# Performance work log

Hardware: AMD Instinct MI355X
Metric: run time of the kernel (lower is better)

The kernel has to match this reference:

```python
import jax, jax.numpy as jnp
import numpy as np

SEQ, BATCH, D_MODEL = 2048, 2, 1024
NHEAD = 16
HEAD_DIM = D_MODEL // NHEAD
D_FF = 4096
LN_EPS = 1e-5
ROPE_THETA = 10000.0


def _rope_cos_sin(seq_len, dim, dtype):
    # lucidrains RotaryEmbedding: inv_freq over even indices, interleaved repeat
    inv_freq = 1.0 / (ROPE_THETA ** (jnp.arange(0, dim, 2, dtype=jnp.float32) / dim))
    t = jnp.arange(seq_len, dtype=jnp.float32)
    freqs = t[:, None] * inv_freq[None, :]            # [S, dim/2]
    freqs = jnp.repeat(freqs, 2, axis=-1)             # [S, dim] (f0,f0,f1,f1,...)
    return jnp.cos(freqs).astype(dtype), jnp.sin(freqs).astype(dtype)


def _rotate_half(x):
    # interleaved pairs: (x0,x1,x2,x3,...) -> (-x1,x0,-x3,x2,...)
    x = x.reshape(x.shape[:-1] + (-1, 2))
    x1, x2 = x[..., 0], x[..., 1]
    return jnp.stack([-x2, x1], axis=-1).reshape(x.shape[:-2] + (-1,))


def _apply_rope(x, cos, sin):
    # x: [B, H, S, D]; cos/sin: [S, D]
    return x * cos[None, None, :, :] + _rotate_half(x) * sin[None, None, :, :]


def _layer_norm(x, g, b):
    mu = jnp.mean(x, axis=-1, keepdims=True)
    var = jnp.mean(jnp.square(x - mu), axis=-1, keepdims=True)
    return (x - mu) * jax.lax.rsqrt(var + LN_EPS) * g + b


def setup_inputs() -> dict:
    key = jax.random.key(0)
    ks = jax.random.split(key, 12)
    s = 1.0 / np.sqrt(D_MODEL)
    sf = 1.0 / np.sqrt(D_FF)
    return {
        "src": jax.random.normal(ks[0], (SEQ, BATCH, D_MODEL), jnp.float32),
        "q_w": jax.random.uniform(ks[1], (D_MODEL, D_MODEL), jnp.float32, -s, s),
        "q_b": jnp.zeros((D_MODEL,), jnp.float32),
        "k_w": jax.random.uniform(ks[2], (D_MODEL, D_MODEL), jnp.float32, -s, s),
        "k_b": jnp.zeros((D_MODEL,), jnp.float32),
        "v_w": jax.random.uniform(ks[3], (D_MODEL, D_MODEL), jnp.float32, -s, s),
        "v_b": jnp.zeros((D_MODEL,), jnp.float32),
        "w1": jax.random.uniform(ks[4], (D_MODEL, D_FF), jnp.float32, -s, s),
        "b1": jnp.zeros((D_FF,), jnp.float32),
        "w2": jax.random.uniform(ks[5], (D_FF, D_MODEL), jnp.float32, -sf, sf),
        "b2": jnp.zeros((D_MODEL,), jnp.float32),
        "ln1_g": jnp.ones((D_MODEL,), jnp.float32),
        "ln1_b": jnp.zeros((D_MODEL,), jnp.float32),
        "ln2_g": jnp.ones((D_MODEL,), jnp.float32),
        "ln2_b": jnp.zeros((D_MODEL,), jnp.float32),
    }


def reference(src, q_w, q_b, k_w, k_b, v_w, v_b, w1, b1, w2, b2,
              ln1_g, ln1_b, ln2_g, ln2_b):
    S, B, E = src.shape
    q = src @ q_w + q_b
    k = src @ k_w + k_b
    v = src @ v_w + v_b
    # [S,B,E] -> [B,H,S,D]
    def split_heads(x):
        return x.reshape(S, B, NHEAD, HEAD_DIM).transpose(1, 2, 0, 3)
    q, k, v = split_heads(q), split_heads(k), split_heads(v)
    cos, sin = _rope_cos_sin(S, HEAD_DIM, src.dtype)
    q = _apply_rope(q, cos, sin)
    k = _apply_rope(k, cos, sin)
    scores = jnp.einsum("bhqd,bhkd->bhqk", q, k) / np.sqrt(HEAD_DIM)
    probs = jax.nn.softmax(scores, axis=-1)
    out = jnp.einsum("bhqk,bhkd->bhqd", probs, v)      # [B,H,S,D]
    out = out.transpose(2, 0, 1, 3).reshape(S, B, E)
    x = _layer_norm(src + out, ln1_g, ln1_b)
    ff = (jax.nn.relu(x @ w1 + b1)) @ w2 + b2
    return _layer_norm(x + ff, ln2_g, ln2_b)
```

## Files before the change

### kernel.cpp

```cpp
#include <hip/hip_runtime.h>
#include <hip/hip_bf16.h>

#define SEQ 2048
#define BATCH 2
#define DMODEL 1024
#define NHEAD 16
#define HDIM 64
#define DFF 4096
#define LN_EPS 1e-5f
#define QKVSZ (BATCH * NHEAD * SEQ * HDIM)

typedef unsigned short ushort_t;
typedef __attribute__((ext_vector_type(8))) short short8;
typedef __attribute__((ext_vector_type(4))) float floatx4;

__device__ __forceinline__ float bf2f(ushort_t u) {
    union { unsigned int i; float f; } v;
    v.i = ((unsigned int)u) << 16;
    return v.f;
}
__device__ __forceinline__ ushort_t f2bf(float f) {
    union { float f; unsigned int i; } v;
    v.f = f;
    unsigned int r = v.i + 0x7fffu + ((v.i >> 16) & 1u);
    return (ushort_t)(r >> 16);
}
__device__ __forceinline__ void gload_lds16(const ushort_t* g, ushort_t* l) {
    __builtin_amdgcn_global_load_lds(
        (const __attribute__((address_space(1))) void*)g,
        (__attribute__((address_space(3))) void*)l, 16, 0, 0);
}

__global__ __launch_bounds__(256) void sniff_kernel(const ushort_t* __restrict__ qw,
                                                    int* __restrict__ flag) {
    float mx = 0.f;
    for (int i = threadIdx.x; i < 4096; i += 256) {
        float v = fabsf(bf2f(qw[i]));
        if (v <= 3.0e38f) mx = fmaxf(mx, v);
    }
#pragma unroll
    for (int off = 1; off < 64; off <<= 1) mx = fmaxf(mx, __shfl_xor(mx, off, 64));
    __shared__ float sm[4];
    if ((threadIdx.x & 63) == 0) sm[threadIdx.x >> 6] = mx;
    __syncthreads();
    if (threadIdx.x == 0) {
        float m = fmaxf(fmaxf(sm[0], sm[1]), fmaxf(sm[2], sm[3]));
        *flag = (m > 1.0f) ? 1 : 0;
    }
}

__global__ __launch_bounds__(256) void convert_kernel(const void* __restrict__ src,
                                                      ushort_t* __restrict__ dst,
                                                      int n, const int* __restrict__ flag) {
    const int f = *flag;
    int i = blockIdx.x * 256 + threadIdx.x;
    const int stride = gridDim.x * 256;
    if (f) {
        const float* s = (const float*)src;
        for (; i < n; i += stride) dst[i] = f2bf(s[i]);
    } else {
        const ushort_t* s = (const ushort_t*)src;
        for (; i < n; i += stride) dst[i] = s[i];
    }
}

__global__ __launch_bounds__(256) void transpose_all_kernel(
    const void* __restrict__ s0, const void* __restrict__ s1,
    const void* __restrict__ s2, const void* __restrict__ s3,
    const void* __restrict__ s4,
    ushort_t* __restrict__ wqkvT, ushort_t* __restrict__ w1T,
    ushort_t* __restrict__ w2T, const int* __restrict__ flag)
{
    __shared__ ushort_t tile[64][72];
    const int id = blockIdx.x;
    const void* src; ushort_t* dst; int K, N, bx, by;
    if (id < 768) {
        int mat = id >> 8, t = id & 255;
        src = (mat == 0) ? s0 : ((mat == 1) ? s1 : s2);
        dst = wqkvT + (size_t)mat * DMODEL * DMODEL;
        K = DMODEL; N = DMODEL; bx = t & 15; by = t >> 4;
    } else if (id < 1792) {
        int t = id - 768;
        src = s3; dst = w1T; K = DMODEL; N = DFF; bx = t & 63; by = t >> 6;
    } else {
        int t = id - 1792;
        src = s4; dst = w2T; K = DFF; N = DMODEL; bx = t & 15; by = t >> 4;
    }
    const int n0 = bx * 64, k0 = by * 64;
    const int tx = threadIdx.x & 63, ty = threadIdx.x >> 6;
    const int f = *flag;
    if (f) {
        const float* s = (const float*)src;
#pragma unroll
        for (int i = 0; i < 16; i++) {
            int r = ty + 4 * i;
            tile[r][tx] = f2bf(s[(size_t)(k0 + r) * N + n0 + tx]);
        }
    } else {
        const ushort_t* s = (const ushort_t*)src;
#pragma unroll
        for (int i = 0; i < 16; i++) {
            int r = ty + 4 * i;
            tile[r][tx] = s[(size_t)(k0 + r) * N + n0 + tx];
        }
    }
    __syncthreads();
#pragma unroll
    for (int i = 0; i < 16; i++) {
        int r = ty + 4 * i;
        dst[(size_t)(n0 + r) * K + k0 + tx] = tile[tx][r];
    }
}

__global__ __launch_bounds__(256) void small_setup_kernel(
    const void* __restrict__ qb, const void* __restrict__ kb,
    const void* __restrict__ vb, const void* __restrict__ b1,
    const void* __restrict__ b2, const void* __restrict__ g1,
    const void* __restrict__ be1, const void* __restrict__ g2,
    const void* __restrict__ be2,
    char* __restrict__ sp, float* __restrict__ rope,
    const int* __restrict__ flag)
{
    const int i = blockIdx.x * 256 + threadIdx.x;
    if (i >= 12288) {
        int idx = i - 12288;
        int s = idx >> 5, ii = idx & 31;
        float inv = exp2f(-(float)(2 * ii) * (13.287712379549449f / 64.f));
        float ang = (float)s * inv;
        rope[idx * 2 + 0] = cosf(ang);
        rope[idx * 2 + 1] = sinf(ang);
        return;
    }
    const int f = *flag;
    const void* src; ushort_t* dst; int j;
    if (i < 3072)       { src = (i < 1024) ? qb : ((i < 2048) ? kb : vb);
                          j = i & 1023; dst = (ushort_t*)sp + i; }
    else if (i < 7168)  { src = b1;  j = i - 3072;  dst = (ushort_t*)(sp + 8192) + j; }
    else if (i < 8192)  { src = b2;  j = i - 7168;  dst = (ushort_t*)(sp + 16384) + j; }
    else if (i < 9216)  { src = g1;  j = i - 8192;  dst = (ushort_t*)(sp + 20480) + j; }
    else if (i < 10240) { src = be1; j = i - 9216;  dst = (ushort_t*)(sp + 24576) + j; }
    else if (i < 11264) { src = g2;  j = i - 10240; dst = (ushort_t*)(sp + 28672) + j; }
    else                { src = be2; j = i - 11264; dst = (ushort_t*)(sp + 32768) + j; }
    *dst = f ? f2bf(((const float*)src)[j]) : ((const ushort_t*)src)[j];
}

template <int MODE>
__global__ __launch_bounds__(256) void gemm_kernel(
    const ushort_t* __restrict__ A, const ushort_t* __restrict__ BT,
    const ushort_t* __restrict__ bias, void* __restrict__ out,
    void* __restrict__ out2, const float* __restrict__ rope,
    int M, int N, int K)
{
    __shared__ ushort_t sA[128 * 32];
    __shared__ ushort_t sB[128 * 32];

    const int tid = threadIdx.x;
    const int lane = tid & 63;
    const int w = tid >> 6;
    const int wm = (w >> 1) * 64;
    const int wn = (w & 1) * 64;
    const int m0 = blockIdx.y * 128;
    const int n0 = blockIdx.x * 128;

    const int Kc = (MODE == 3) ? (K >> 1) : K;
    const int kbeg = (MODE == 3) ? (int)blockIdx.z * Kc : 0;

    floatx4 acc[4][4];
#pragma unroll
    for (int i = 0; i < 4; i++)
#pragma unroll
        for (int j = 0; j < 4; j++) {
            floatx4 z = {0.f, 0.f, 0.f, 0.f};
            acc[i][j] = z;
        }

    const int srow = tid >> 2;
    const int scol = (tid & 3) * 8;
    const ushort_t* Ag = A + (size_t)(m0 + srow) * K + scol + kbeg;
    const ushort_t* Bg = BT + (size_t)(n0 + srow) * K + scol + kbeg;
    ushort_t* ldsA0 = sA + w * 512;
    ushort_t* ldsA1 = sA + 2048 + w * 512;
    ushort_t* ldsB0 = sB + w * 512;
    ushort_t* ldsB1 = sB + 2048 + w * 512;
    const size_t rstep = (size_t)64 * K;

    for (int k0 = 0; k0 < Kc; k0 += 32) {
        gload_lds16(Ag + k0, ldsA0);
        gload_lds16(Ag + rstep + k0, ldsA1);
        gload_lds16(Bg + k0, ldsB0);
        gload_lds16(Bg + rstep + k0, ldsB1);
        __syncthreads();

        short8 a[4], b[4];
#pragma unroll
        for (int mt = 0; mt < 4; mt++)
            a[mt] = *(const short8*)&sA[(wm + mt * 16 + (lane & 15)) * 32 + (lane >> 4) * 8];
#pragma unroll
        for (int nt = 0; nt < 4; nt++)
            b[nt] = *(const short8*)&sB[(wn + nt * 16 + (lane & 15)) * 32 + (lane >> 4) * 8];
#pragma unroll
        for (int mt = 0; mt < 4; mt++)
#pragma unroll
            for (int nt = 0; nt < 4; nt++)
                acc[mt][nt] = __builtin_amdgcn_mfma_f32_16x16x32_bf16(
                    a[mt], b[nt], acc[mt][nt], 0, 0, 0);
        __syncthreads();
    }

#pragma unroll
    for (int mt = 0; mt < 4; mt++) {
#pragma unroll
        for (int nt = 0; nt < 4; nt++) {
#pragma unroll
            for (int r = 0; r < 4; r++) {
                int row = wm + mt * 16 + (lane >> 4) * 4 + r;
                int col = wn + nt * 16 + (lane & 15);
                int m = m0 + row, n = n0 + col;
                float val = acc[mt][nt][r];
                if (MODE != 3) val += bf2f(bias[n]);
                if (MODE == 1) {
                    int mat = n >> 10, nn = n & 1023;
                    int h = nn >> 6, d = nn & 63;
                    int s = m >> 1, bb = m & 1;
                    if (mat < 2) {
                        int i = d >> 1;
                        float c  = rope[((size_t)s * 32 + i) * 2 + 0];
                        float sn = rope[((size_t)s * 32 + i) * 2 + 1];
                        float partner = __shfl_xor(val, 1, 64);
                        val = (d & 1) ? (val * c + partner * sn)
                                      : (val * c - partner * sn);
                        if (mat == 0) val *= 0.18033688011112042f;
                    }
                    size_t off;
                    if (mat == 2)
                        off = (size_t)2 * QKVSZ + ((size_t)(bb * NHEAD + h) * HDIM + d) * SEQ + s;
                    else
                        off = (size_t)mat * QKVSZ + ((size_t)(bb * NHEAD + h) * SEQ + s) * HDIM + d;
                    ((ushort_t*)out)[off] = f2bf(val);
                } else if (MODE == 2) {
                    ((ushort_t*)out)[(size_t)m * N + n] = f2bf(fmaxf(val, 0.f));
                } else {
                    float* outp = blockIdx.z ? (float*)out2 : (float*)out;
                    outp[(size_t)m * N + n] = val;
                }
            }
        }
    }
}

__global__ __launch_bounds__(256) void attn_kernel(
    const ushort_t* __restrict__ Q, const ushort_t* __restrict__ K,
    const ushort_t* __restrict__ VT, ushort_t* __restrict__ out)
{
    __shared__ ushort_t sQ[128][72];
    __shared__ ushort_t sK[64][72];
    __shared__ ushort_t sVT[64][72];
    __shared__ ushort_t sP[128][72];

    const int tid = threadIdx.x;
    const int lane = tid & 63;
    const int w = tid >> 6;
    const int quad = lane >> 4;
    const int l15 = lane & 15;
    const int bh = blockIdx.y;
    const int q0 = blockIdx.x * 128;

    const ushort_t* Qg  = Q + ((size_t)bh * SEQ + q0) * HDIM;
    const ushort_t* Kg  = K + (size_t)bh * SEQ * HDIM;
    const ushort_t* VTg = VT + (size_t)bh * SEQ * HDIM;

#pragma unroll
    for (int p = 0; p < 4; p++) {
        int chunk = tid + p * 256;
        int r = chunk >> 3, c = (chunk & 7) * 8;
        *(short8*)&sQ[r][c] = *(const short8*)(Qg + (size_t)r * HDIM + c);
    }
    __syncthreads();
    short8 aQ[2][2];
#pragma unroll
    for (int mt = 0; mt < 2; mt++)
#pragma unroll
        for (int kk = 0; kk < 2; kk++)
            aQ[mt][kk] = *(const short8*)&sQ[w * 32 + mt * 16 + l15][kk * 32 + quad * 8];

    floatx4 accO[2][4];
    floatx4 accL[2];
#pragma unroll
    for (int mt = 0; mt < 2; mt++) {
        floatx4 z = {0.f, 0.f, 0.f, 0.f};
        accL[mt] = z;
#pragma unroll
        for (int nt = 0; nt < 4; nt++) accO[mt][nt] = z;
    }
    short8 ones;
#pragma unroll
    for (int j = 0; j < 8; j++) ones[j] = (short)0x3F80;

    for (int kv0 = 0; kv0 < SEQ; kv0 += 64) {
        __syncthreads();
#pragma unroll
        for (int p = 0; p < 2; p++) {
            int chunk = tid + p * 256;
            int r = chunk >> 3, c = (chunk & 7) * 8;
            *(short8*)&sK[r][c]  = *(const short8*)(Kg + (size_t)(kv0 + r) * HDIM + c);
            *(short8*)&sVT[r][c] = *(const short8*)(VTg + (size_t)r * SEQ + kv0 + c);
        }
        __syncthreads();

        floatx4 accS[2][4];
#pragma unroll
        for (int mt = 0; mt < 2; mt++)
#pragma unroll
            for (int nt = 0; nt < 4; nt++) {
                floatx4 z = {0.f, 0.f, 0.f, 0.f};
                accS[mt][nt] = z;
            }
#pragma unroll
        for (int kk = 0; kk < 2; kk++)
#pragma unroll
            for (int nt = 0; nt < 4; nt++) {
                short8 bK = *(const short8*)&sK[nt * 16 + l15][kk * 32 + quad * 8];
#pragma unroll
                for (int mt = 0; mt < 2; mt++)
                    accS[mt][nt] = __builtin_amdgcn_mfma_f32_16x16x32_bf16(
                        aQ[mt][kk], bK, accS[mt][nt], 0, 0, 0);
            }

#pragma unroll
        for (int mt = 0; mt < 2; mt++)
#pragma unroll
            for (int nt = 0; nt < 4; nt++)
#pragma unroll
                for (int r = 0; r < 4; r++)
                    sP[w * 32 + mt * 16 + quad * 4 + r][nt * 16 + l15] =
                        f2bf(exp2f(accS[mt][nt][r]));

#pragma unroll
        for (int mt = 0; mt < 2; mt++) {
#pragma unroll
            for (int kkp = 0; kkp < 2; kkp++) {
                short8 aP = *(const short8*)&sP[w * 32 + mt * 16 + l15][kkp * 32 + quad * 8];
#pragma unroll
                for (int nt = 0; nt < 4; nt++) {
                    short8 bV = *(const short8*)&sVT[nt * 16 + l15][kkp * 32 + quad * 8];
                    accO[mt][nt] = __builtin_amdgcn_mfma_f32_16x16x32_bf16(
                        aP, bV, accO[mt][nt], 0, 0, 0);
                }
                accL[mt] = __builtin_amdgcn_mfma_f32_16x16x32_bf16(
                    aP, ones, accL[mt], 0, 0, 0);
            }
        }
    }

    const int b = bh >> 4, h = bh & 15;
#pragma unroll
    for (int mt = 0; mt < 2; mt++) {
        float rinv[4];
#pragma unroll
        for (int r = 0; r < 4; r++) rinv[r] = 1.0f / accL[mt][r];
#pragma unroll
        for (int nt = 0; nt < 4; nt++)
#pragma unroll
            for (int r = 0; r < 4; r++) {
                int qrow = q0 + w * 32 + mt * 16 + quad * 4 + r;
                int d = nt * 16 + l15;
                out[((size_t)qrow * BATCH + b) * DMODEL + h * HDIM + d] =
                    f2bf(accO[mt][nt][r] * rinv[r]);
            }
    }
}

__global__ __launch_bounds__(256) void ln1_kernel(
    const ushort_t* __restrict__ src, ushort_t* io,
    const ushort_t* __restrict__ g, const ushort_t* __restrict__ bb)
{
    const int row = blockIdx.x;
    const int tid = threadIdx.x;
    const size_t base = (size_t)row * DMODEL;
    const int j0 = tid * 4;
    float v[4];
#pragma unroll
    for (int j = 0; j < 4; j++)
        v[j] = bf2f(src[base + j0 + j]) + bf2f(io[base + j0 + j]);

    float s = v[0] + v[1] + v[2] + v[3];
    float ss = v[0] * v[0] + v[1] * v[1] + v[2] * v[2] + v[3] * v[3];
#pragma unroll
    for (int off = 1; off < 64; off <<= 1) {
        s += __shfl_xor(s, off, 64);
        ss += __shfl_xor(ss, off, 64);
    }
    __shared__ float ps[4], pss[4];
    if ((tid & 63) == 0) { ps[tid >> 6] = s; pss[tid >> 6] = ss; }
    __syncthreads();
    s = ps[0] + ps[1] + ps[2] + ps[3];
    ss = pss[0] + pss[1] + pss[2] + pss[3];
    float mu = s * (1.f / DMODEL);
    float var = ss * (1.f / DMODEL) - mu * mu;
    float rstd = rsqrtf(var + LN_EPS);
#pragma unroll
    for (int j = 0; j < 4; j++) {
        float y = (v[j] - mu) * rstd * bf2f(g[j0 + j]) + bf2f(bb[j0 + j]);
        io[base + j0 + j] = f2bf(y);
    }
}

__global__ __launch_bounds__(256) void ln2_kernel(
    const ushort_t* __restrict__ xb, float* io,
    const float* __restrict__ ff1, const ushort_t* __restrict__ b2,
    const ushort_t* __restrict__ g, const ushort_t* __restrict__ bb)
{
    const int row = blockIdx.x;
    const int tid = threadIdx.x;
    const size_t base = (size_t)row * DMODEL;
    const int j0 = tid * 4;
    float v[4];
#pragma unroll
    for (int j = 0; j < 4; j++)
        v[j] = bf2f(xb[base + j0 + j]) + io[base + j0 + j] + ff1[base + j0 + j]
             + bf2f(b2[j0 + j]);

    float s = v[0] + v[1] + v[2] + v[3];
    float ss = v[0] * v[0] + v[1] * v[1] + v[2] * v[2] + v[3] * v[3];
#pragma unroll
    for (int off = 1; off < 64; off <<= 1) {
        s += __shfl_xor(s, off, 64);
        ss += __shfl_xor(ss, off, 64);
    }
    __shared__ float ps[4], pss[4];
    if ((tid & 63) == 0) { ps[tid >> 6] = s; pss[tid >> 6] = ss; }
    __syncthreads();
    s = ps[0] + ps[1] + ps[2] + ps[3];
    ss = pss[0] + pss[1] + pss[2] + pss[3];
    float mu = s * (1.f / DMODEL);
    float var = ss * (1.f / DMODEL) - mu * mu;
    float rstd = rsqrtf(var + LN_EPS);
#pragma unroll
    for (int j = 0; j < 4; j++) {
        float y = (v[j] - mu) * rstd * bf2f(g[j0 + j]) + bf2f(bb[j0 + j]);
        io[base + j0 + j] = y;
    }
}

extern "C" void kernel_launch(void* const* d_in, const int* in_sizes, int n_in,
                              void* d_out, int out_size, void* d_ws, size_t ws_size,
                              hipStream_t stream)
{
    char* ws = (char*)d_ws;
    const size_t MB = 1024 * 1024;
    const size_t KB = 1024;

    ushort_t* c_src   = (ushort_t*)(ws + 0);
    ushort_t* c_wqkvT = (ushort_t*)(ws + 8 * MB);
    ushort_t* c_w1T   = (ushort_t*)(ws + 14 * MB);
    ushort_t* c_w2T   = (ushort_t*)(ws + 22 * MB);
    char* sp = ws + 30 * MB;
    ushort_t* c_qkvb  = (ushort_t*)(sp + 0 * KB);
    ushort_t* c_b1    = (ushort_t*)(sp + 8 * KB);
    ushort_t* c_b2    = (ushort_t*)(sp + 16 * KB);
    ushort_t* c_ln1g  = (ushort_t*)(sp + 20 * KB);
    ushort_t* c_ln1b  = (ushort_t*)(sp + 24 * KB);
    ushort_t* c_ln2g  = (ushort_t*)(sp + 28 * KB);
    ushort_t* c_ln2b  = (ushort_t*)(sp + 32 * KB);
    int*      flag    = (int*)(sp + 36 * KB);
    float*    rope    = (float*)(ws + 30 * MB + 512 * KB);
    ushort_t* QKVb    = (ushort_t*)(ws + 31 * MB);
    ushort_t* attn_xb = (ushort_t*)(ws + 63 * MB);
    ushort_t* hbuf    = (ushort_t*)(ws + 31 * MB);
    float*    ffb1    = (float*)(ws + 0);
    float*    ffb0    = (float*)d_out;

    const int M = SEQ * BATCH;
    dim3 blk(256);

    sniff_kernel<<<dim3(1), blk, 0, stream>>>((const ushort_t*)d_in[1], flag);

    transpose_all_kernel<<<dim3(2816), blk, 0, stream>>>(
        d_in[1], d_in[3], d_in[5], d_in[7], d_in[9],
        c_wqkvT, c_w1T, c_w2T, flag);

    convert_kernel<<<dim3(2048), blk, 0, stream>>>(
        d_in[0], c_src, SEQ * BATCH * DMODEL, flag);

    small_setup_kernel<<<dim3(304), blk, 0, stream>>>(
        d_in[2], d_in[4], d_in[6], d_in[8], d_in[10],
        d_in[11], d_in[12], d_in[13], d_in[14],
        sp, rope, flag);

    gemm_kernel<1><<<dim3(3 * DMODEL / 128, M / 128), blk, 0, stream>>>(
        c_src, c_wqkvT, c_qkvb, QKVb, nullptr, rope, M, 3 * DMODEL, DMODEL);

    attn_kernel<<<dim3(SEQ / 128, BATCH * NHEAD), blk, 0, stream>>>(
        QKVb, QKVb + QKVSZ, QKVb + 2 * QKVSZ, attn_xb);

    ln1_kernel<<<dim3(M), blk, 0, stream>>>(c_src, attn_xb, c_ln1g, c_ln1b);

    gemm_kernel<2><<<dim3(DFF / 128, M / 128), blk, 0, stream>>>(
        attn_xb, c_w1T, c_b1, hbuf, nullptr, rope, M, DFF, DMODEL);

    gemm_kernel<3><<<dim3(DMODEL / 128, M / 128, 2), blk, 0, stream>>>(
        hbuf, c_w2T, c_b2, ffb0, ffb1, rope, M, DMODEL, DFF);

    ln2_kernel<<<dim3(M), blk, 0, stream>>>(attn_xb, ffb0, ffb1, c_b2, c_ln2g, c_ln2b);
}
```

Before: 400.5 us.

## Rework attention to 32x32 MFMA with in-register P via permlane swap

The attention kernel moves from 16x16x32 to 32x32x16 MFMAs and computes S transposed (K as A operand, Q as B operand), so each lane holds one query column of P. P is packed to bf16 with v_cvt_pk_bf16_f32 and reshuffled with v_permlane32_swap to feed the PV MFMA directly, which removes the sP shared-memory round trip. The row sum is accumulated with scalar adds instead of an extra MFMA against a ones vector. Output is staged through shared memory for coalesced 16-byte stores. This adds reliance on gfx950-specific instructions and on an exact register layout, which is a correctness risk if the layout is wrong.

New measurement: 394.7 us. No clear change (-1.5%).

```diff
diff --git a/kernel.cpp b/kernel.cpp
--- a/kernel.cpp
+++ b/kernel.cpp
@@ -13,6 +13,7 @@
 typedef unsigned short ushort_t;
 typedef __attribute__((ext_vector_type(8))) short short8;
 typedef __attribute__((ext_vector_type(4))) float floatx4;
+typedef __attribute__((ext_vector_type(16))) float floatx16;
 
 __device__ __forceinline__ float bf2f(ushort_t u) {
     union { unsigned int i; float f; } v;
@@ -24,6 +25,11 @@
     v.f = f;
     unsigned int r = v.i + 0x7fffu + ((v.i >> 16) & 1u);
     return (ushort_t)(r >> 16);
+}
+__device__ __forceinline__ unsigned int cvtpk_bf16(float lo, float hi) {
+    unsigned int r;
+    asm("v_cvt_pk_bf16_f32 %0, %1, %2" : "=v"(r) : "v"(lo), "v"(hi));
+    return r;
 }
 __device__ __forceinline__ void gload_lds16(const ushort_t* g, ushort_t* l) {
     __builtin_amdgcn_global_load_lds(
@@ -252,18 +258,17 @@
     const ushort_t* __restrict__ Q, const ushort_t* __restrict__ K,
     const ushort_t* __restrict__ VT, ushort_t* __restrict__ out)
 {
-    __shared__ ushort_t sQ[128][72];
+    __shared__ ushort_t sQO[128][72];
     __shared__ ushort_t sK[64][72];
     __shared__ ushort_t sVT[64][72];
-    __shared__ ushort_t sP[128][72];
-
-    const int tid = threadIdx.x;
+
+    const int tid  = threadIdx.x;
     const int lane = tid & 63;
-    const int w = tid >> 6;
-    const int quad = lane >> 4;
-    const int l15 = lane & 15;
-    const int bh = blockIdx.y;
-    const int q0 = blockIdx.x * 128;
+    const int w    = tid >> 6;
+    const int h    = lane >> 5;
+    const int q5   = lane & 31;
+    const int bh   = blockIdx.y;
+    const int q0   = blockIdx.x * 128;
 
     const ushort_t* Qg  = Q + ((size_t)bh * SEQ + q0) * HDIM;
     const ushort_t* Kg  = K + (size_t)bh * SEQ * HDIM;
@@ -273,28 +278,21 @@
     for (int p = 0; p < 4; p++) {
         int chunk = tid + p * 256;
         int r = chunk >> 3, c = (chunk & 7) * 8;
-        *(short8*)&sQ[r][c] = *(const short8*)(Qg + (size_t)r * HDIM + c);
+        *(short8*)&sQO[r][c] = *(const short8*)(Qg + (size_t)r * HDIM + c);
     }
     __syncthreads();
-    short8 aQ[2][2];
-#pragma unroll
-    for (int mt = 0; mt < 2; mt++)
-#pragma unroll
-        for (int kk = 0; kk < 2; kk++)
-            aQ[mt][kk] = *(const short8*)&sQ[w * 32 + mt * 16 + l15][kk * 32 + quad * 8];
-
-    floatx4 accO[2][4];
-    floatx4 accL[2];
-#pragma unroll
-    for (int mt = 0; mt < 2; mt++) {
-        floatx4 z = {0.f, 0.f, 0.f, 0.f};
-        accL[mt] = z;
-#pragma unroll
-        for (int nt = 0; nt < 4; nt++) accO[mt][nt] = z;
-    }
-    short8 ones;
-#pragma unroll
-    for (int j = 0; j < 8; j++) ones[j] = (short)0x3F80;
+
+    short8 qf[4];
+#pragma unroll
+    for (int kk = 0; kk < 4; kk++)
+        qf[kk] = *(const short8*)&sQO[w * 32 + q5][kk * 16 + h * 8];
+
+    floatx16 accO[2];
+#pragma unroll
+    for (int dt = 0; dt < 2; dt++)
+#pragma unroll
+        for (int r = 0; r < 16; r++) accO[dt][r] = 0.f;
+    float accL = 0.f;
 
     for (int kv0 = 0; kv0 < SEQ; kv0 += 64) {
         __syncthreads();
@@ -307,66 +305,71 @@
         }
         __syncthreads();
 
-        floatx4 accS[2][4];
-#pragma unroll
-        for (int mt = 0; mt < 2; mt++)
-#pragma unroll
-            for (int nt = 0; nt < 4; nt++) {
-                floatx4 z = {0.f, 0.f, 0.f, 0.f};
-                accS[mt][nt] = z;
+        floatx16 accS[2];
+#pragma unroll
+        for (int t = 0; t < 2; t++) {
+#pragma unroll
+            for (int r = 0; r < 16; r++) accS[t][r] = 0.f;
+#pragma unroll
+            for (int kk = 0; kk < 4; kk++) {
+                short8 aK = *(const short8*)&sK[t * 32 + q5][kk * 16 + h * 8];
+                accS[t] = __builtin_amdgcn_mfma_f32_32x32x16_bf16(
+                    aK, qf[kk], accS[t], 0, 0, 0);
             }
-#pragma unroll
-        for (int kk = 0; kk < 2; kk++)
-#pragma unroll
-            for (int nt = 0; nt < 4; nt++) {
-                short8 bK = *(const short8*)&sK[nt * 16 + l15][kk * 32 + quad * 8];
-#pragma unroll
-                for (int mt = 0; mt < 2; mt++)
-                    accS[mt][nt] = __builtin_amdgcn_mfma_f32_16x16x32_bf16(
-                        aQ[mt][kk], bK, accS[mt][nt], 0, 0, 0);
+        }
+
+        unsigned int pa[2][4], pb[2][4];
+#pragma unroll
+        for (int t = 0; t < 2; t++) {
+#pragma unroll
+            for (int r = 0; r < 16; r++) {
+                accS[t][r] = exp2f(accS[t][r]);
+                accL += accS[t][r];
             }
-
-#pragma unroll
-        for (int mt = 0; mt < 2; mt++)
-#pragma unroll
-            for (int nt = 0; nt < 4; nt++)
-#pragma unroll
-                for (int r = 0; r < 4; r++)
-                    sP[w * 32 + mt * 16 + quad * 4 + r][nt * 16 + l15] =
-                        f2bf(exp2f(accS[mt][nt][r]));
-
-#pragma unroll
-        for (int mt = 0; mt < 2; mt++) {
-#pragma unroll
-            for (int kkp = 0; kkp < 2; kkp++) {
-                short8 aP = *(const short8*)&sP[w * 32 + mt * 16 + l15][kkp * 32 + quad * 8];
-#pragma unroll
-                for (int nt = 0; nt < 4; nt++) {
-                    short8 bV = *(const short8*)&sVT[nt * 16 + l15][kkp * 32 + quad * 8];
-                    accO[mt][nt] = __builtin_amdgcn_mfma_f32_16x16x32_bf16(
-                        aP, bV, accO[mt][nt], 0, 0, 0);
-                }
-                accL[mt] = __builtin_amdgcn_mfma_f32_16x16x32_bf16(
-                    aP, ones, accL[mt], 0, 0, 0);
+#pragma unroll
+            for (int s = 0; s < 4; s++) {
+                pa[t][s] = cvtpk_bf16(accS[t][4 * s + 0], accS[t][4 * s + 1]);
+                pb[t][s] = cvtpk_bf16(accS[t][4 * s + 2], accS[t][4 * s + 3]);
             }
         }
-    }
-
-    const int b = bh >> 4, h = bh & 15;
-#pragma unroll
-    for (int mt = 0; mt < 2; mt++) {
-        float rinv[4];
-#pragma unroll
-        for (int r = 0; r < 4; r++) rinv[r] = 1.0f / accL[mt][r];
-#pragma unroll
-        for (int nt = 0; nt < 4; nt++)
-#pragma unroll
-            for (int r = 0; r < 4; r++) {
-                int qrow = q0 + w * 32 + mt * 16 + quad * 4 + r;
-                int d = nt * 16 + l15;
-                out[((size_t)qrow * BATCH + b) * DMODEL + h * HDIM + d] =
-                    f2bf(accO[mt][nt][r] * rinv[r]);
+
+#pragma unroll
+        for (int w4 = 0; w4 < 4; w4++) {
+            const int t = w4 >> 1, wh = w4 & 1;
+            unsigned int xa = pa[t][2 * wh + 1], ya = pa[t][2 * wh];
+            unsigned int xb = pb[t][2 * wh + 1], yb = pb[t][2 * wh];
+            asm volatile("v_permlane32_swap_b32 %0, %1" : "+v"(xa), "+v"(ya));
+            asm volatile("v_permlane32_swap_b32 %0, %1" : "+v"(xb), "+v"(yb));
+            union { unsigned int u[4]; short8 s; } bf;
+            bf.u[0] = ya; bf.u[1] = yb; bf.u[2] = xa; bf.u[3] = xb;
+#pragma unroll
+            for (int dt = 0; dt < 2; dt++) {
+                short8 aV = *(const short8*)&sVT[dt * 32 + q5][w4 * 16 + h * 8];
+                accO[dt] = __builtin_amdgcn_mfma_f32_32x32x16_bf16(
+                    aV, bf.s, accO[dt], 0, 0, 0);
             }
+        }
+    }
+
+    accL += __shfl_xor(accL, 32, 64);
+    float rinv = 1.0f / accL;
+
+#pragma unroll
+    for (int dt = 0; dt < 2; dt++)
+#pragma unroll
+        for (int r = 0; r < 16; r++) {
+            int d = dt * 32 + (r & 3) + 8 * (r >> 2) + 4 * h;
+            sQO[w * 32 + q5][d] = f2bf(accO[dt][r] * rinv);
+        }
+
+    const int b = bh >> 4, hd = bh & 15;
+#pragma unroll
+    for (int p = 0; p < 4; p++) {
+        int rl = p * 8 + (lane >> 3);
+        int c = (lane & 7) * 8;
+        int qrow = q0 + w * 32 + rl;
+        short8 v = *(const short8*)&sQO[w * 32 + rl][c];
+        *(short8*)(out + ((size_t)qrow * BATCH + b) * DMODEL + hd * HDIM + c) = v;
     }
 }
 
```
